# Kernel tuning notes

Hardware: AMD Instinct MI355X
Metric: run time of the kernel (lower is better)

Reference implementation:

```python
import jax, jax.numpy as jnp
import numpy as np

N, A, R = 131072, 16, 64


def setup_inputs() -> dict:
    key = jax.random.key(0)
    k1, k2, k3 = jax.random.split(key, 3)
    x = jax.random.normal(k1, (N, A), dtype=jnp.float32)
    mu = jax.random.uniform(k2, (R, A), dtype=jnp.float32)      # torch.rand(R, A)
    sigma = jnp.ones((R, A), dtype=jnp.float32) * 0.2           # torch.ones(R, A) * 0.2
    rho = jax.random.normal(k3, (R, A + 1), dtype=jnp.float32) * 0.1
    return {"x": x, "mu": mu, "sigma": sigma, "rho": rho}


def reference(x, mu, sigma, rho):
    # Rule consequents: z[k, r] = x[k] . rho[r, :A] + rho[r, A]   -> [N, R]
    z = jnp.einsum("na,ra->nr", x, rho[:, :-1]) + rho[:, -1]
    # Gaussian membership firing strengths (prod of exps == exp of sum):
    # w[k, r] = prod_a exp(-(x[k,a]-mu[r,a])^2 / (2 sigma[r,a]^2))
    d = x[:, None, :] - mu[None, :, :]                           # [N, R, A]
    logw = -jnp.sum(d * d / (2.0 * sigma[None] ** 2), axis=-1)   # [N, R]
    w = jnp.exp(logw)
    # diag(z @ w.T)[k] = sum_r z[k,r] * w[k,r]; normalized by rule-sum.
    num = jnp.sum(z * w, axis=1)
    den = jnp.sum(w, axis=1) + 1e-13
    return num / den
```

## Files before the change

### kernel.cpp

```cpp
#include <hip/hip_runtime.h>
#include <math.h>

#define NFEAT 16
#define NRULE 64
#define ROWDW 80
#define FLAG_DW (64 * ROWDW)

typedef _Float16 half8 __attribute__((ext_vector_type(8)));
typedef float    f4    __attribute__((ext_vector_type(4)));
union F4H8 { float4 f; half8 h; };

__global__ void fuzzy_prep(const float* __restrict__ mu,
                           const float* __restrict__ sigma,
                           const float* __restrict__ rho,
                           float* __restrict__ tab) {
    const float L2E = 1.4426950408889634f;
    __shared__ int u_sh[256];
    int t = threadIdx.x;
    int L = t & 63, T = t >> 6;
    int n = L & 15, quad = L >> 4;
    int rule = T * 16 + n;
    int fb = (quad & 1) * 8;

    F4H8 b1, b2, r1, r2;
#pragma unroll
    for (int j = 0; j < 8; ++j) {
        int f = fb + j;
        float m = mu[rule * NFEAT + f];
        float s = sigma[rule * NFEAT + f];
        float inv = 1.0f / (2.0f * s * s);
        float Bw = 2.0f * inv * m * L2E;
        _Float16 bh = (_Float16)Bw;
        b1.h[j] = bh;
        b2.h[j] = (_Float16)(Bw - (float)bh);
        float Rw = rho[rule * (NFEAT + 1) + f];
        _Float16 rh = (_Float16)Rw;
        r1.h[j] = rh;
        r2.h[j] = (_Float16)(Rw - (float)rh);
    }
    float* rowp = tab + L * ROWDW;
    ((float4*)rowp)[T]      = b1.f;
    ((float4*)rowp)[4 + T]  = b2.f;
    ((float4*)rowp)[8 + T]  = r1.f;
    ((float4*)rowp)[12 + T] = r2.f;

    float s0 = sigma[rule * NFEAT];
    float c0 = 1.0f / (2.0f * s0 * s0);
    float K = 0.0f;
    int u = 1;
#pragma unroll
    for (int a = 0; a < NFEAT; ++a) {
        float m = mu[rule * NFEAT + a];
        float s = sigma[rule * NFEAT + a];
        float inv = 1.0f / (2.0f * s * s);
        if (inv != c0) u = 0;
        K = fmaf(-inv * m, m, K);
    }
    rowp[64 + T] = -c0 * L2E;
    rowp[68 + T] = K * L2E;
    rowp[72 + T] = rho[rule * (NFEAT + 1) + NFEAT];

    u_sh[t] = u;
    __syncthreads();
    if (t < 64) {
        int uu = u_sh[t] & u_sh[t + 64] & u_sh[t + 128] & u_sh[t + 192];
        unsigned long long b = __ballot(uu != 0);
        if (t == 0) tab[FLAG_DW] = (b == ~0ull) ? 1.0f : 0.0f;
    }
}

__global__ __launch_bounds__(256, 4) void fuzzy_main(const float* __restrict__ x,
                                                     const float* __restrict__ tab,
                                                     const float* __restrict__ mu,
                                                     const float* __restrict__ sigma,
                                                     const float* __restrict__ rho,
                                                     float* __restrict__ out, int n) {
    const int tid  = threadIdx.x;
    const int L    = tid & 63;
    const int quad = L >> 4;
    const int wv   = __builtin_amdgcn_readfirstlane(tid >> 6);
    const int flag = __builtin_amdgcn_readfirstlane((int)tab[FLAG_DW]);
    const int m    = L & 15;
    const int fb   = (quad & 1) * 8;

    if (flag) {
        const float4* row = (const float4*)(tab + L * ROWDW);
        F4H8 b1[4], b2[4], r1[4], r2[4];
#pragma unroll
        for (int T = 0; T < 4; ++T) {
            b1[T].f = row[T];      b2[T].f = row[4 + T];
            r1[T].f = row[8 + T];  r2[T].f = row[12 + T];
        }
        float4 Pq = row[16], Kq = row[17], Bq = row[18];
        float PvA[4]  = {Pq.x, Pq.y, Pq.z, Pq.w};
        float KLvA[4] = {Kq.x, Kq.y, Kq.z, Kq.w};
        float BvA[4]  = {Bq.x, Bq.y, Bq.z, Bq.w};

#pragma unroll
        for (int it = 0; it < 2; ++it) {
            int gt = (blockIdx.x * 4 + wv) * 2 + it;
            int tb = gt * 16;
            if (tb >= n) break;
            const float4* xp = (const float4*)(x + (size_t)(tb + m) * NFEAT + fb);
            float4 xa = xp[0], xb = xp[1];
            float xv[8] = {xa.x, xa.y, xa.z, xa.w, xb.x, xb.y, xb.z, xb.w};
            F4H8 af;
            float qp = 0.0f;
#pragma unroll
            for (int j = 0; j < 8; ++j) {
                _Float16 h = (_Float16)xv[j];
                af.h[j] = (quad < 2) ? h : (_Float16)(xv[j] - (float)h);
                qp = fmaf(xv[j], xv[j], qp);
            }
            float Qf = qp + __shfl_xor(qp, 16);
            float Qr[4];
#pragma unroll
            for (int p = 0; p < 4; ++p) Qr[p] = __shfl(Qf, quad * 4 + p);

            f4 nsum = {0.f, 0.f, 0.f, 0.f}, dsum = {0.f, 0.f, 0.f, 0.f};
#pragma unroll
            for (int T = 0; T < 4; ++T) {
                f4 z4 = {0.f, 0.f, 0.f, 0.f};
                f4 accL = __builtin_amdgcn_mfma_f32_16x16x32_f16(af.h, b1[T].h, z4, 0, 0, 0);
                accL    = __builtin_amdgcn_mfma_f32_16x16x32_f16(af.h, b2[T].h, accL, 0, 0, 0);
                f4 accZ = __builtin_amdgcn_mfma_f32_16x16x32_f16(af.h, r1[T].h, z4, 0, 0, 0);
                accZ    = __builtin_amdgcn_mfma_f32_16x16x32_f16(af.h, r2[T].h, accZ, 0, 0, 0);
#pragma unroll
                for (int p = 0; p < 4; ++p) {
                    float l = fmaf(PvA[T], Qr[p], accL[p] + KLvA[T]);
                    float w = __builtin_amdgcn_exp2f(l);
                    float zf = accZ[p] + BvA[T];
                    nsum[p] = fmaf(zf, w, nsum[p]);
                    dsum[p] += w;
                }
            }
#pragma unroll
            for (int d = 1; d < 16; d <<= 1) {
#pragma unroll
                for (int p = 0; p < 4; ++p) {
                    nsum[p] += __shfl_xor(nsum[p], d);
                    dsum[p] += __shfl_xor(dsum[p], d);
                }
            }
            if ((L & 15) == 0) {
                float4 o;
                o.x = nsum[0] * __builtin_amdgcn_rcpf(dsum[0] + 1e-13f);
                o.y = nsum[1] * __builtin_amdgcn_rcpf(dsum[1] + 1e-13f);
                o.z = nsum[2] * __builtin_amdgcn_rcpf(dsum[2] + 1e-13f);
                o.w = nsum[3] * __builtin_amdgcn_rcpf(dsum[3] + 1e-13f);
                ((float4*)(out + tb))[quad] = o;
            }
        }
    } else {
        const float L2E = 1.4426950408889634f;
#pragma unroll
        for (int it = 0; it < 2; ++it) {
            int gt = (blockIdx.x * 4 + wv) * 2 + it;
            int tb = gt * 16;
            if (tb >= n) break;
            int s = tb + m;
            const float4* xp = (const float4*)(x + (size_t)s * NFEAT);
            float4 a = xp[0], b = xp[1], c = xp[2], d = xp[3];
            float xs[NFEAT] = {a.x,a.y,a.z,a.w, b.x,b.y,b.z,b.w,
                               c.x,c.y,c.z,c.w, d.x,d.y,d.z,d.w};
            float num = 0.0f, den = 0.0f;
            for (int r = quad * 16; r < quad * 16 + 16; ++r) {
                float z = rho[r * (NFEAT + 1) + NFEAT];
                float l = 0.0f;
                for (int aa = 0; aa < NFEAT; ++aa) {
                    float mm = mu[r * NFEAT + aa];
                    float ss = sigma[r * NFEAT + aa];
                    float inv = 1.0f / (2.0f * ss * ss);
                    float dd = xs[aa] - mm;
                    l = fmaf(-inv * dd, dd, l);
                    z = fmaf(rho[r * (NFEAT + 1) + aa], xs[aa], z);
                }
                float w = __builtin_amdgcn_exp2f(l * L2E);
                num = fmaf(z, w, num);
                den += w;
            }
            num += __shfl_xor(num, 16); den += __shfl_xor(den, 16);
            num += __shfl_xor(num, 32); den += __shfl_xor(den, 32);
            if (L < 16) out[tb + L] = num / (den + 1e-13f);
        }
    }
}

extern "C" void kernel_launch(void* const* d_in, const int* in_sizes, int n_in,
                              void* d_out, int out_size, void* d_ws, size_t ws_size,
                              hipStream_t stream) {
    const float* x     = (const float*)d_in[0];
    const float* mu    = (const float*)d_in[1];
    const float* sigma = (const float*)d_in[2];
    const float* rho   = (const float*)d_in[3];
    float* out = (float*)d_out;
    float* tab = (float*)d_ws;

    int n = in_sizes[0] / NFEAT;

    fuzzy_prep<<<1, 256, 0, stream>>>(mu, sigma, rho, tab);
    int blocks = (n + 127) / 128;
    fuzzy_main<<<blocks, 256, 0, stream>>>(x, tab, mu, sigma, rho, out, n);
}
```

Measured before the change: 70.17 us.

## Fuse parameter prep into main kernel and prefetch x before table build

Removes the single-block prep kernel and its workspace table. Every wave now rebuilds the split-fp16 MFMA operands, constants and uniform-sigma flag from mu/sigma/rho in registers, using a wave ballot in place of the cross-block flag. The x tiles are loaded before this setup so their global latency overlaps with the parameter math. This saves a launch and the serial dependency between kernels, at the cost of redundant per-wave divides and parameter loads.

```diff
diff --git a/kernel.cpp b/kernel.cpp
--- a/kernel.cpp
+++ b/kernel.cpp
@@ -3,107 +3,76 @@
 
 #define NFEAT 16
 #define NRULE 64
-#define ROWDW 80
-#define FLAG_DW (64 * ROWDW)
+#define TPW 2
 
 typedef _Float16 half8 __attribute__((ext_vector_type(8)));
 typedef float    f4    __attribute__((ext_vector_type(4)));
 union F4H8 { float4 f; half8 h; };
 
-__global__ void fuzzy_prep(const float* __restrict__ mu,
-                           const float* __restrict__ sigma,
-                           const float* __restrict__ rho,
-                           float* __restrict__ tab) {
+__global__ __launch_bounds__(256, 4) void fuzzy_fused(const float* __restrict__ x,
+                                                      const float* __restrict__ mu,
+                                                      const float* __restrict__ sigma,
+                                                      const float* __restrict__ rho,
+                                                      float* __restrict__ out, int n) {
     const float L2E = 1.4426950408889634f;
-    __shared__ int u_sh[256];
-    int t = threadIdx.x;
-    int L = t & 63, T = t >> 6;
-    int n = L & 15, quad = L >> 4;
-    int rule = T * 16 + n;
-    int fb = (quad & 1) * 8;
-
-    F4H8 b1, b2, r1, r2;
-#pragma unroll
-    for (int j = 0; j < 8; ++j) {
-        int f = fb + j;
-        float m = mu[rule * NFEAT + f];
-        float s = sigma[rule * NFEAT + f];
-        float inv = 1.0f / (2.0f * s * s);
-        float Bw = 2.0f * inv * m * L2E;
-        _Float16 bh = (_Float16)Bw;
-        b1.h[j] = bh;
-        b2.h[j] = (_Float16)(Bw - (float)bh);
-        float Rw = rho[rule * (NFEAT + 1) + f];
-        _Float16 rh = (_Float16)Rw;
-        r1.h[j] = rh;
-        r2.h[j] = (_Float16)(Rw - (float)rh);
-    }
-    float* rowp = tab + L * ROWDW;
-    ((float4*)rowp)[T]      = b1.f;
-    ((float4*)rowp)[4 + T]  = b2.f;
-    ((float4*)rowp)[8 + T]  = r1.f;
-    ((float4*)rowp)[12 + T] = r2.f;
-
-    float s0 = sigma[rule * NFEAT];
-    float c0 = 1.0f / (2.0f * s0 * s0);
-    float K = 0.0f;
-    int u = 1;
-#pragma unroll
-    for (int a = 0; a < NFEAT; ++a) {
-        float m = mu[rule * NFEAT + a];
-        float s = sigma[rule * NFEAT + a];
-        float inv = 1.0f / (2.0f * s * s);
-        if (inv != c0) u = 0;
-        K = fmaf(-inv * m, m, K);
-    }
-    rowp[64 + T] = -c0 * L2E;
-    rowp[68 + T] = K * L2E;
-    rowp[72 + T] = rho[rule * (NFEAT + 1) + NFEAT];
-
-    u_sh[t] = u;
-    __syncthreads();
-    if (t < 64) {
-        int uu = u_sh[t] & u_sh[t + 64] & u_sh[t + 128] & u_sh[t + 192];
-        unsigned long long b = __ballot(uu != 0);
-        if (t == 0) tab[FLAG_DW] = (b == ~0ull) ? 1.0f : 0.0f;
-    }
-}
-
-__global__ __launch_bounds__(256, 4) void fuzzy_main(const float* __restrict__ x,
-                                                     const float* __restrict__ tab,
-                                                     const float* __restrict__ mu,
-                                                     const float* __restrict__ sigma,
-                                                     const float* __restrict__ rho,
-                                                     float* __restrict__ out, int n) {
     const int tid  = threadIdx.x;
     const int L    = tid & 63;
     const int quad = L >> 4;
+    const int m    = L & 15;
     const int wv   = __builtin_amdgcn_readfirstlane(tid >> 6);
-    const int flag = __builtin_amdgcn_readfirstlane((int)tab[FLAG_DW]);
-    const int m    = L & 15;
     const int fb   = (quad & 1) * 8;
 
+    const int tbase = (blockIdx.x * 4 + wv) * TPW;
+    float4 xa[TPW], xb[TPW];
+#pragma unroll
+    for (int t = 0; t < TPW; ++t) {
+        int tb = (tbase + t) * 16;
+        int sc = tb + m < n ? tb + m : n - 1;
+        const float4* xp = (const float4*)(x + (size_t)sc * NFEAT + fb);
+        xa[t] = xp[0]; xb[t] = xp[1];
+    }
+
+    F4H8 b1[4], b2[4], r1[4], r2[4];
+    float Pv[4], KLv[4], Bv[4];
+    bool u = true;
+#pragma unroll
+    for (int T = 0; T < 4; ++T) {
+        int rule = T * 16 + m;
+        const float* mrow = mu    + rule * NFEAT + fb;
+        const float* srow = sigma + rule * NFEAT + fb;
+        const float* rrow = rho   + rule * (NFEAT + 1) + fb;
+        float s0 = sigma[rule * NFEAT];
+        float c0 = 1.0f / (2.0f * s0 * s0);
+        float kp = 0.0f;
+#pragma unroll
+        for (int j = 0; j < 8; ++j) {
+            float mm = mrow[j], ss = srow[j];
+            float inv = 1.0f / (2.0f * ss * ss);
+            u = u && (inv == c0);
+            float Bw = 2.0f * inv * mm * L2E;
+            _Float16 bh = (_Float16)Bw;
+            b1[T].h[j] = bh;
+            b2[T].h[j] = (_Float16)(Bw - (float)bh);
+            float Rw = rrow[j];
+            _Float16 rh_ = (_Float16)Rw;
+            r1[T].h[j] = rh_;
+            r2[T].h[j] = (_Float16)(Rw - (float)rh_);
+            kp = fmaf(-inv * mm, mm, kp);
+        }
+        Pv[T]  = -c0 * L2E;
+        KLv[T] = (kp + __shfl_xor(kp, 16)) * L2E;
+        Bv[T]  = rho[rule * (NFEAT + 1) + NFEAT];
+    }
+    const int flag =
+        __builtin_amdgcn_readfirstlane((int)(__ballot(u) == ~0ull));
+
     if (flag) {
-        const float4* row = (const float4*)(tab + L * ROWDW);
-        F4H8 b1[4], b2[4], r1[4], r2[4];
 #pragma unroll
-        for (int T = 0; T < 4; ++T) {
-            b1[T].f = row[T];      b2[T].f = row[4 + T];
-            r1[T].f = row[8 + T];  r2[T].f = row[12 + T];
-        }
-        float4 Pq = row[16], Kq = row[17], Bq = row[18];
-        float PvA[4]  = {Pq.x, Pq.y, Pq.z, Pq.w};
-        float KLvA[4] = {Kq.x, Kq.y, Kq.z, Kq.w};
-        float BvA[4]  = {Bq.x, Bq.y, Bq.z, Bq.w};
-
-#pragma unroll
-        for (int it = 0; it < 2; ++it) {
-            int gt = (blockIdx.x * 4 + wv) * 2 + it;
-            int tb = gt * 16;
+        for (int t = 0; t < TPW; ++t) {
+            int tb = (tbase + t) * 16;
             if (tb >= n) break;
-            const float4* xp = (const float4*)(x + (size_t)(tb + m) * NFEAT + fb);
-            float4 xa = xp[0], xb = xp[1];
-            float xv[8] = {xa.x, xa.y, xa.z, xa.w, xb.x, xb.y, xb.z, xb.w};
+            float xv[8] = {xa[t].x, xa[t].y, xa[t].z, xa[t].w,
+                           xb[t].x, xb[t].y, xb[t].z, xb[t].w};
             F4H8 af;
             float qp = 0.0f;
 #pragma unroll
@@ -127,9 +96,9 @@
                 accZ    = __builtin_amdgcn_mfma_f32_16x16x32_f16(af.h, r2[T].h, accZ, 0, 0, 0);
 #pragma unroll
                 for (int p = 0; p < 4; ++p) {
-                    float l = fmaf(PvA[T], Qr[p], accL[p] + KLvA[T]);
+                    float l = fmaf(Pv[T], Qr[p], accL[p] + KLv[T]);
                     float w = __builtin_amdgcn_exp2f(l);
-                    float zf = accZ[p] + BvA[T];
+                    float zf = accZ[p] + Bv[T];
                     nsum[p] = fmaf(zf, w, nsum[p]);
                     dsum[p] += w;
                 }
@@ -142,7 +111,7 @@
                     dsum[p] += __shfl_xor(dsum[p], d);
                 }
             }
-            if ((L & 15) == 0) {
+            if (m == 0) {
                 float4 o;
                 o.x = nsum[0] * __builtin_amdgcn_rcpf(dsum[0] + 1e-13f);
                 o.y = nsum[1] * __builtin_amdgcn_rcpf(dsum[1] + 1e-13f);
@@ -152,11 +121,9 @@
             }
         }
     } else {
-        const float L2E = 1.4426950408889634f;
 #pragma unroll
-        for (int it = 0; it < 2; ++it) {
-            int gt = (blockIdx.x * 4 + wv) * 2 + it;
-            int tb = gt * 16;
+        for (int t = 0; t < TPW; ++t) {
+            int tb = (tbase + t) * 16;
             if (tb >= n) break;
             int s = tb + m;
             const float4* xp = (const float4*)(x + (size_t)s * NFEAT);
@@ -194,11 +161,9 @@
     const float* sigma = (const float*)d_in[2];
     const float* rho   = (const float*)d_in[3];
     float* out = (float*)d_out;
-    float* tab = (float*)d_ws;
 
     int n = in_sizes[0] / NFEAT;
 
-    fuzzy_prep<<<1, 256, 0, stream>>>(mu, sigma, rho, tab);
-    int blocks = (n + 127) / 128;
-    fuzzy_main<<<blocks, 256, 0, stream>>>(x, tab, mu, sigma, rho, out, n);
+    int blocks = (n + 16 * 4 * TPW - 1) / (16 * 4 * TPW);
+    fuzzy_fused<<<blocks, 256, 0, stream>>>(x, mu, sigma, rho, out, n);
 }
```

New measurement: 79.17 us. +12.8%, slower.
